# Performance work log

Hardware: AMD Instinct MI355X
Metric: run time of the kernel (lower is better)

## Reference

```python
import jax, jax.numpy as jnp
import numpy as np

PENALTY_LAMBDA = 0.5
MAX_RULES = 512
INIT_GATE_LOGIT = -2.0


def setup_inputs() -> dict:
    key = jax.random.key(0)
    k1, k2, k3 = jax.random.split(key, 3)
    B, V, E = 64, 128000, 1000000
    logits = jax.random.normal(k1, (B, V), dtype=jnp.float32)
    # learned per-rule gate logits (nn.Parameter initialized at init_gate_logit;
    # we perturb slightly so gradients are non-degenerate)
    gate_logits = jnp.full((MAX_RULES,), INIT_GATE_LOGIT, dtype=jnp.float32) \
        + 0.1 * jax.random.normal(k2, (MAX_RULES,), dtype=jnp.float32)
    # flattened ragged (rule, token) violation pairs
    kr, kt = jax.random.split(k3)
    rule_ids = jax.random.randint(kr, (E,), 0, MAX_RULES, dtype=jnp.int32)
    token_ids = jax.random.randint(kt, (E,), 0, V, dtype=jnp.int32)
    return {"logits": logits, "gate_logits": gate_logits,
            "rule_ids": rule_ids, "token_ids": token_ids}


def reference(logits, gate_logits, rule_ids, token_ids):
    # eval-mode binary concrete gate (no noise, no thresholding): sigmoid(logit)
    gates = jax.nn.sigmoid(gate_logits)                      # [R]
    V = logits.shape[-1]
    # gated penalty value per (rule, token) pair, single vectorized scatter-add
    vals = gates[rule_ids] * jnp.asarray(PENALTY_LAMBDA, logits.dtype)  # [E]
    pen_1d = jnp.zeros((V,), dtype=logits.dtype).at[token_ids].add(vals)  # [V]
    penalties = jnp.broadcast_to(pen_1d[None, :], logits.shape)           # [B,V]
    modified = logits - penalties
    # coverage loss: -mean of gates over rules that fire (have >=1 violation)
    firing = jnp.zeros((MAX_RULES,), dtype=logits.dtype).at[rule_ids].set(1.0)
    n_firing = jnp.maximum(firing.sum(), 1.0)
    coverage_loss = -(gates * firing).sum() / n_firing
    return modified, coverage_loss, penalties
```

## Files before the change

### kernel.cpp

```cpp
#include <hip/hip_runtime.h>

#define PENALTY_LAMBDA 0.5f
#define RULES 512
#define NR 4
#define RS 32000
#define VOCAB 128000
#define G 64
#define NB 64
#define CH 500
#define CJ 125

typedef float    f32x4 __attribute__((ext_vector_type(4)));
typedef _Float16 f16x4 __attribute__((ext_vector_type(4)));


__global__ void __launch_bounds__(1024) scatter_kernel(
    const int* __restrict__ rule_ids, const int* __restrict__ token_ids,
    const float* __restrict__ gate_logits, _Float16* __restrict__ partials,
    unsigned* __restrict__ masks, int E) {
    __shared__ __align__(16) float hist[RS];
    __shared__ float s_g[RULES];
    __shared__ unsigned char s_f[RULES];
    int t = threadIdx.x;
    int g = blockIdx.x;
    int r = blockIdx.y;
    for (int i = t * 4; i < RS; i += 1024 * 4)
        *(f32x4*)(hist + i) = (f32x4){0.f, 0.f, 0.f, 0.f};
    if (t < RULES) {
        float x = gate_logits[t];
        s_g[t] = PENALTY_LAMBDA / (1.0f + expf(-x));
    }
    if (t >= 512 && t < 512 + RULES / 4) ((unsigned*)s_f)[t - 512] = 0u;
    __syncthreads();

    const int lo = r * RS;
    const int stride = G * 1024 * 4;
    for (int base = (g * 1024 + t) * 4; base + 4 <= E; base += stride) {
        int4 tt = *(const int4*)(token_ids + base);
        int4 rr = *(const int4*)(rule_ids + base);
        int ts[4] = {tt.x, tt.y, tt.z, tt.w};
        int rv[4] = {rr.x, rr.y, rr.z, rr.w};
#pragma unroll
        for (int k = 0; k < 4; ++k) {
            int tok = ts[k] - lo;
            if ((unsigned)tok < (unsigned)RS)
                unsafeAtomicAdd(&hist[tok], s_g[rv[k]]);
            if (r == 0) s_f[rv[k]] = 1;
        }
    }
    if (g == 0 && t == 0) {
        for (int e = E & ~3; e < E; ++e) {
            int tok = token_ids[e] - lo; int ru = rule_ids[e];
            if ((unsigned)tok < (unsigned)RS)
                unsafeAtomicAdd(&hist[tok], s_g[ru]);
            if (r == 0) s_f[ru] = 1;
        }
    }
    __syncthreads();

    _Float16* dst = partials + ((size_t)r * G + g) * RS;
    for (int i = t * 4; i < RS; i += 1024 * 4) {
        f32x4 s = *(const f32x4*)(&hist[i]);
        f16x4 h = {(_Float16)s.x, (_Float16)s.y, (_Float16)s.z, (_Float16)s.w};
        *(f16x4*)(dst + i) = h;
    }

    if (r == 0 && t < 16) {
        const unsigned* w = (const unsigned*)s_f + t * 8;
        unsigned m = 0;
#pragma unroll
        for (int k = 0; k < 8; ++k) {
            unsigned d = w[k];
            if (d & 0x000000FFu) m |= 1u << (k * 4 + 0);
            if (d & 0x0000FF00u) m |= 1u << (k * 4 + 1);
            if (d & 0x00FF0000u) m |= 1u << (k * 4 + 2);
            if (d & 0xFF000000u) m |= 1u << (k * 4 + 3);
        }
        masks[g * 16 + t] = m;
    }
}

__global__ void __launch_bounds__(512) fused_kernel(
    const _Float16* __restrict__ partials, const unsigned* __restrict__ masks,
    const float* __restrict__ gate_logits, const float* __restrict__ logits,
    float* __restrict__ out_mod, float* __restrict__ out_pen,
    float* __restrict__ out_loss) {
    __shared__ float s_pc[CH + 4];
    __shared__ f32x4 s_part[4][CJ + 1];
    int t = threadIdx.x;
    int tx = t & 127, ty = t >> 7;
    int chunk = blockIdx.x;
    int c0 = chunk * CH;
    int r = c0 / RS;
    int bin = c0 - r * RS;

    {
        if (tx < CJ) {
            f32x4 acc = {0.f, 0.f, 0.f, 0.f};
            const _Float16* bp = partials + ((size_t)r * G + ty * 16) * RS
                               + bin + tx * 4;
#pragma unroll 4
            for (int g = 0; g < 16; ++g) {
                f16x4 h = *(const f16x4*)(bp + (size_t)g * RS);
                acc += (f32x4){(float)h.x, (float)h.y, (float)h.z, (float)h.w};
            }
            s_part[ty][tx] = acc;
        } else if (tx == 127) {
            f32x4 e = {0.f, 0.f, 0.f, 0.f};
            for (int i = 0; i < 4; ++i) {
                int gb = c0 + CH + i; if (gb >= VOCAB) gb -= VOCAB;
                int r2 = gb / RS, b2 = gb - r2 * RS;
                const _Float16* bp2 = partials + ((size_t)r2 * G + ty * 16) * RS + b2;
                float s = 0.f;
                for (int g = 0; g < 16; ++g) s += (float)bp2[(size_t)g * RS];
                ((float*)&e)[i] = s;
            }
            s_part[ty][CJ] = e;
        }
    }
    __syncthreads();
    if (t < CJ + 1) {
        f32x4 s = s_part[0][t] + s_part[1][t] + s_part[2][t] + s_part[3][t];
        *(f32x4*)(s_pc + t * 4) = s;
    }
    __syncthreads();

    if (chunk == 0) {
        __shared__ unsigned s_mask[16];
        __shared__ float sg[8], sf[8];
        if (t < 16) {
            unsigned m = 0;
            for (int g = 0; g < G; ++g) m |= masks[g * 16 + t];
            s_mask[t] = m;
        }
        __syncthreads();
        float f = ((s_mask[t >> 5] >> (t & 31)) & 1u) ? 1.f : 0.f;
        float gf = f / (1.f + expf(-gate_logits[t]));
        for (int off = 32; off > 0; off >>= 1) {
            gf += __shfl_down(gf, off, 64);
            f  += __shfl_down(f,  off, 64);
        }
        if ((t & 63) == 0) { sg[t >> 6] = gf; sf[t >> 6] = f; }
        __syncthreads();
        if (t == 0) {
            float tg = 0.f, tf = 0.f;
            for (int w = 0; w < 8; ++w) { tg += sg[w]; tf += sf[w]; }
            *out_loss = -tg / fmaxf(tf, 1.0f);
            out_pen[0] = s_pc[0];
            out_pen[1] = s_pc[1];
            out_pen[2] = s_pc[2];
        }
    }

    if (tx >= CJ) return;
    f32x4 p0 = *(const f32x4*)(s_pc + tx * 4);
    f32x4 ps = {s_pc[tx * 4 + 3], s_pc[tx * 4 + 4],
                s_pc[tx * 4 + 5], s_pc[tx * 4 + 6]};
    bool glast = (chunk == 255 && tx == CJ - 1);
    size_t col = (size_t)c0 + tx * 4;
#pragma unroll 4
    for (int ib = 0; ib < NB / 4; ++ib) {
        int b = ib * 4 + ty;
        size_t base = (size_t)b * VOCAB + col;
        f32x4 l = __builtin_nontemporal_load((const f32x4*)(logits + base));
        __builtin_nontemporal_store(l - p0, (f32x4*)(out_mod + base));
        if (glast && b == NB - 1) {
            out_pen[base + 3] = p0.w;
        } else {
            __builtin_nontemporal_store(ps, (f32x4*)(out_pen + base + 3));
        }
    }
}

extern "C" void kernel_launch(void* const* d_in, const int* in_sizes, int n_in,
                              void* d_out, int out_size, void* d_ws, size_t ws_size,
                              hipStream_t stream) {
    const float* logits      = (const float*)d_in[0];
    const float* gate_logits = (const float*)d_in[1];
    const int*   rule_ids    = (const int*)d_in[2];
    const int*   token_ids   = (const int*)d_in[3];
    float* out = (float*)d_out;

    const int E = in_sizes[2];
    const size_t BV = (size_t)NB * VOCAB;

    _Float16* partials = (_Float16*)d_ws;
    unsigned* masks    = (unsigned*)(partials + (size_t)NR * G * RS);

    scatter_kernel<<<dim3(G, NR), 1024, 0, stream>>>(
        rule_ids, token_ids, gate_logits, partials, masks, E);

    fused_kernel<<<VOCAB / CH, 512, 0, stream>>>(
        partials, masks, gate_logits, logits,
        out, out + BV + 1, out + BV);
}
```

Baseline: 122.8 us.

## Merge scatter and fused kernels into one cooperative kernel with grid sync

```diff
diff --git a/kernel.cpp b/kernel.cpp
--- a/kernel.cpp
+++ b/kernel.cpp
@@ -1,4 +1,7 @@
 #include <hip/hip_runtime.h>
+#include <hip/hip_cooperative_groups.h>
+
+namespace cg = cooperative_groups;
 
 #define PENALTY_LAMBDA 0.5f
 #define RULES 512
@@ -13,134 +16,135 @@
 typedef float    f32x4 __attribute__((ext_vector_type(4)));
 typedef _Float16 f16x4 __attribute__((ext_vector_type(4)));
 
-
-__global__ void __launch_bounds__(1024) scatter_kernel(
+__global__ void __launch_bounds__(1024) mega_kernel(
     const int* __restrict__ rule_ids, const int* __restrict__ token_ids,
-    const float* __restrict__ gate_logits, _Float16* __restrict__ partials,
-    unsigned* __restrict__ masks, int E) {
-    __shared__ __align__(16) float hist[RS];
-    __shared__ float s_g[RULES];
-    __shared__ unsigned char s_f[RULES];
+    const float* __restrict__ gate_logits, const float* __restrict__ logits,
+    _Float16* __restrict__ partials, unsigned* __restrict__ masks,
+    float* __restrict__ out_mod, float* __restrict__ out_pen,
+    float* __restrict__ out_loss, int E) {
+    __shared__ __align__(16) float lds[32640];
+    __shared__ unsigned s_mask[16];
+    __shared__ float sg[8], sf[8];
     int t = threadIdx.x;
-    int g = blockIdx.x;
-    int r = blockIdx.y;
-    for (int i = t * 4; i < RS; i += 1024 * 4)
-        *(f32x4*)(hist + i) = (f32x4){0.f, 0.f, 0.f, 0.f};
-    if (t < RULES) {
-        float x = gate_logits[t];
-        s_g[t] = PENALTY_LAMBDA / (1.0f + expf(-x));
-    }
-    if (t >= 512 && t < 512 + RULES / 4) ((unsigned*)s_f)[t - 512] = 0u;
-    __syncthreads();
-
-    const int lo = r * RS;
-    const int stride = G * 1024 * 4;
-    for (int base = (g * 1024 + t) * 4; base + 4 <= E; base += stride) {
-        int4 tt = *(const int4*)(token_ids + base);
-        int4 rr = *(const int4*)(rule_ids + base);
-        int ts[4] = {tt.x, tt.y, tt.z, tt.w};
-        int rv[4] = {rr.x, rr.y, rr.z, rr.w};
-#pragma unroll
-        for (int k = 0; k < 4; ++k) {
-            int tok = ts[k] - lo;
-            if ((unsigned)tok < (unsigned)RS)
-                unsafeAtomicAdd(&hist[tok], s_g[rv[k]]);
-            if (r == 0) s_f[rv[k]] = 1;
-        }
-    }
-    if (g == 0 && t == 0) {
-        for (int e = E & ~3; e < E; ++e) {
-            int tok = token_ids[e] - lo; int ru = rule_ids[e];
-            if ((unsigned)tok < (unsigned)RS)
-                unsafeAtomicAdd(&hist[tok], s_g[ru]);
-            if (r == 0) s_f[ru] = 1;
-        }
-    }
-    __syncthreads();
-
-    _Float16* dst = partials + ((size_t)r * G + g) * RS;
-    for (int i = t * 4; i < RS; i += 1024 * 4) {
-        f32x4 s = *(const f32x4*)(&hist[i]);
-        f16x4 h = {(_Float16)s.x, (_Float16)s.y, (_Float16)s.z, (_Float16)s.w};
-        *(f16x4*)(dst + i) = h;
-    }
-
-    if (r == 0 && t < 16) {
-        const unsigned* w = (const unsigned*)s_f + t * 8;
-        unsigned m = 0;
-#pragma unroll
-        for (int k = 0; k < 8; ++k) {
-            unsigned d = w[k];
-            if (d & 0x000000FFu) m |= 1u << (k * 4 + 0);
-            if (d & 0x0000FF00u) m |= 1u << (k * 4 + 1);
-            if (d & 0x00FF0000u) m |= 1u << (k * 4 + 2);
-            if (d & 0xFF000000u) m |= 1u << (k * 4 + 3);
-        }
-        masks[g * 16 + t] = m;
-    }
-}
-
-__global__ void __launch_bounds__(512) fused_kernel(
-    const _Float16* __restrict__ partials, const unsigned* __restrict__ masks,
-    const float* __restrict__ gate_logits, const float* __restrict__ logits,
-    float* __restrict__ out_mod, float* __restrict__ out_pen,
-    float* __restrict__ out_loss) {
-    __shared__ float s_pc[CH + 4];
-    __shared__ f32x4 s_part[4][CJ + 1];
-    int t = threadIdx.x;
+    int bid = blockIdx.x;
+
+    {
+        float* hist = lds;
+        float* s_g  = lds + 32000;
+        unsigned char* s_f = (unsigned char*)(lds + 32512);
+        int g = bid & 63, r = bid >> 6;
+        for (int i = t * 4; i < RS; i += 1024 * 4)
+            *(f32x4*)(hist + i) = (f32x4){0.f, 0.f, 0.f, 0.f};
+        if (t < RULES)
+            s_g[t] = PENALTY_LAMBDA / (1.0f + expf(-gate_logits[t]));
+        if (t >= 512 && t < 512 + RULES / 4) ((unsigned*)s_f)[t - 512] = 0u;
+        __syncthreads();
+
+        const int lo = r * RS;
+        const int stride = G * 1024 * 4;
+        for (int base = (g * 1024 + t) * 4; base + 4 <= E; base += stride) {
+            int4 tt = *(const int4*)(token_ids + base);
+            int4 rr = *(const int4*)(rule_ids + base);
+            int ts[4] = {tt.x, tt.y, tt.z, tt.w};
+            int rv[4] = {rr.x, rr.y, rr.z, rr.w};
+#pragma unroll
+            for (int k = 0; k < 4; ++k) {
+                int tok = ts[k] - lo;
+                if ((unsigned)tok < (unsigned)RS)
+                    unsafeAtomicAdd(&hist[tok], s_g[rv[k]]);
+                if (r == 0) s_f[rv[k]] = 1;
+            }
+        }
+        if (g == 0 && t == 0) {
+            for (int e = E & ~3; e < E; ++e) {
+                int tok = token_ids[e] - lo; int ru = rule_ids[e];
+                if ((unsigned)tok < (unsigned)RS)
+                    unsafeAtomicAdd(&hist[tok], s_g[ru]);
+                if (r == 0) s_f[ru] = 1;
+            }
+        }
+        __syncthreads();
+
+        _Float16* dst = partials + ((size_t)r * G + g) * RS;
+        for (int i = t * 4; i < RS; i += 1024 * 4) {
+            f32x4 s = *(const f32x4*)(&hist[i]);
+            f16x4 h = {(_Float16)s.x, (_Float16)s.y, (_Float16)s.z, (_Float16)s.w};
+            *(f16x4*)(dst + i) = h;
+        }
+        if (r == 0 && t < 16) {
+            const unsigned* w = (const unsigned*)s_f + t * 8;
+            unsigned m = 0;
+#pragma unroll
+            for (int k = 0; k < 8; ++k) {
+                unsigned d = w[k];
+                if (d & 0x000000FFu) m |= 1u << (k * 4 + 0);
+                if (d & 0x0000FF00u) m |= 1u << (k * 4 + 1);
+                if (d & 0x00FF0000u) m |= 1u << (k * 4 + 2);
+                if (d & 0xFF000000u) m |= 1u << (k * 4 + 3);
+            }
+            masks[g * 16 + t] = m;
+        }
+    }
+
+    __threadfence();
+    cg::this_grid().sync();
+
+    int chunk = bid;
+    int c0 = chunk * CH;
     int tx = t & 127, ty = t >> 7;
-    int chunk = blockIdx.x;
-    int c0 = chunk * CH;
-    int r = c0 / RS;
-    int bin = c0 - r * RS;
-
+    float* s_pc   = lds;
+    f32x4* s_part = (f32x4*)(lds + 512);
     {
+        int r = c0 / RS;
+        int bin = c0 - r * RS;
         if (tx < CJ) {
             f32x4 acc = {0.f, 0.f, 0.f, 0.f};
-            const _Float16* bp = partials + ((size_t)r * G + ty * 16) * RS
+            const _Float16* bp = partials + ((size_t)r * G + ty * 8) * RS
                                + bin + tx * 4;
-#pragma unroll 4
-            for (int g = 0; g < 16; ++g) {
-                f16x4 h = *(const f16x4*)(bp + (size_t)g * RS);
+#pragma unroll
+            for (int gg = 0; gg < 8; ++gg) {
+                f16x4 h = *(const f16x4*)(bp + (size_t)gg * RS);
                 acc += (f32x4){(float)h.x, (float)h.y, (float)h.z, (float)h.w};
             }
-            s_part[ty][tx] = acc;
+            s_part[ty * 126 + tx] = acc;
         } else if (tx == 127) {
             f32x4 e = {0.f, 0.f, 0.f, 0.f};
             for (int i = 0; i < 4; ++i) {
                 int gb = c0 + CH + i; if (gb >= VOCAB) gb -= VOCAB;
                 int r2 = gb / RS, b2 = gb - r2 * RS;
-                const _Float16* bp2 = partials + ((size_t)r2 * G + ty * 16) * RS + b2;
+                const _Float16* bp2 = partials + ((size_t)r2 * G + ty * 8) * RS + b2;
                 float s = 0.f;
-                for (int g = 0; g < 16; ++g) s += (float)bp2[(size_t)g * RS];
+                for (int gg = 0; gg < 8; ++gg) s += (float)bp2[(size_t)gg * RS];
                 ((float*)&e)[i] = s;
             }
-            s_part[ty][CJ] = e;
+            s_part[ty * 126 + CJ] = e;
         }
     }
     __syncthreads();
     if (t < CJ + 1) {
-        f32x4 s = s_part[0][t] + s_part[1][t] + s_part[2][t] + s_part[3][t];
+        f32x4 s = {0.f, 0.f, 0.f, 0.f};
+#pragma unroll
+        for (int j = 0; j < 8; ++j) s += s_part[j * 126 + t];
         *(f32x4*)(s_pc + t * 4) = s;
     }
     __syncthreads();
 
     if (chunk == 0) {
-        __shared__ unsigned s_mask[16];
-        __shared__ float sg[8], sf[8];
         if (t < 16) {
             unsigned m = 0;
-            for (int g = 0; g < G; ++g) m |= masks[g * 16 + t];
+            for (int gg = 0; gg < G; ++gg) m |= masks[gg * 16 + t];
             s_mask[t] = m;
         }
         __syncthreads();
-        float f = ((s_mask[t >> 5] >> (t & 31)) & 1u) ? 1.f : 0.f;
-        float gf = f / (1.f + expf(-gate_logits[t]));
-        for (int off = 32; off > 0; off >>= 1) {
-            gf += __shfl_down(gf, off, 64);
-            f  += __shfl_down(f,  off, 64);
-        }
-        if ((t & 63) == 0) { sg[t >> 6] = gf; sf[t >> 6] = f; }
+        if (t < RULES) {
+            float f = ((s_mask[t >> 5] >> (t & 31)) & 1u) ? 1.f : 0.f;
+            float gf = f / (1.f + expf(-gate_logits[t]));
+            for (int off = 32; off > 0; off >>= 1) {
+                gf += __shfl_down(gf, off, 64);
+                f  += __shfl_down(f,  off, 64);
+            }
+            if ((t & 63) == 0) { sg[t >> 6] = gf; sf[t >> 6] = f; }
+        }
         __syncthreads();
         if (t == 0) {
             float tg = 0.f, tf = 0.f;
@@ -158,9 +162,9 @@
                 s_pc[tx * 4 + 5], s_pc[tx * 4 + 6]};
     bool glast = (chunk == 255 && tx == CJ - 1);
     size_t col = (size_t)c0 + tx * 4;
-#pragma unroll 4
-    for (int ib = 0; ib < NB / 4; ++ib) {
-        int b = ib * 4 + ty;
+#pragma unroll
+    for (int ib = 0; ib < NB / 8; ++ib) {
+        int b = ib * 8 + ty;
         size_t base = (size_t)b * VOCAB + col;
         f32x4 l = __builtin_nontemporal_load((const f32x4*)(logits + base));
         __builtin_nontemporal_store(l - p0, (f32x4*)(out_mod + base));
@@ -181,16 +185,21 @@
     const int*   token_ids   = (const int*)d_in[3];
     float* out = (float*)d_out;
 
-    const int E = in_sizes[2];
+    int E = in_sizes[2];
     const size_t BV = (size_t)NB * VOCAB;
 
     _Float16* partials = (_Float16*)d_ws;
     unsigned* masks    = (unsigned*)(partials + (size_t)NR * G * RS);
 
-    scatter_kernel<<<dim3(G, NR), 1024, 0, stream>>>(
-        rule_ids, token_ids, gate_logits, partials, masks, E);
-
-    fused_kernel<<<VOCAB / CH, 512, 0, stream>>>(
-        partials, masks, gate_logits, logits,
-        out, out + BV + 1, out + BV);
+    float* out_mod  = out;
+    float* out_pen  = out + BV + 1;
+    float* out_loss = out + BV;
+
+    void* kargs[] = {
+        (void*)&rule_ids, (void*)&token_ids, (void*)&gate_logits, (void*)&logits,
+        (void*)&partials, (void*)&masks,
+        (void*)&out_mod, (void*)&out_pen, (void*)&out_loss, (void*)&E
+    };
+    hipLaunchCooperativeKernel((const void*)mega_kernel, dim3(G * NR), dim3(1024),
+                               kargs, 0, stream);
 }
```

Measured after the change: 274.1 us. 123% more time.
